# Kernel optimization log

Hardware: AMD Instinct MI355X
Metric: run time of the kernel (lower is better)

Reference implementation:

```python
import jax, jax.numpy as jnp
import numpy as np

N = 50000   # nodes
E = 800000  # edges
D = 128     # hidden_dim == input_dim
H = 8       # heads
C = D // H  # per-head dim = 16
ED = 10     # edge_dim
FF = 4 * D  # ffn hidden = 512


def setup_inputs() -> dict:
    key = jax.random.key(0)
    ks = jax.random.split(key, 20)
    s = 0.05
    p = lambda k, shape: (jax.random.normal(k, shape, jnp.float32) * s)
    return {
        "x": jax.random.normal(ks[0], (N, D), jnp.float32),
        "edge_index": jax.random.randint(ks[1], (2, E), 0, N),
        "edge_attr": jax.random.normal(ks[2], (E, ED), jnp.float32),
        # TransformerConv params (PyG): lin_query/key/value have bias, lin_edge no bias,
        # lin_skip has bias, lin_beta no bias
        "Wq": p(ks[3], (D, D)), "bq": jnp.zeros((D,), jnp.float32),
        "Wk": p(ks[4], (D, D)), "bk": jnp.zeros((D,), jnp.float32),
        "Wv": p(ks[5], (D, D)), "bv": jnp.zeros((D,), jnp.float32),
        "We": p(ks[6], (ED, D)),
        "Wskip": p(ks[7], (D, D)), "bskip": jnp.zeros((D,), jnp.float32),
        "Wbeta": p(ks[8], (3 * D, 1)),
        # GraphNorm params
        "gn_w": jnp.ones((D,), jnp.float32),
        "gn_b": jnp.zeros((D,), jnp.float32),
        "gn_ms": jnp.ones((D,), jnp.float32),  # mean_scale
        # FFN params
        "W1": p(ks[9], (D, FF)), "b1": jnp.zeros((FF,), jnp.float32),
        "W2": p(ks[10], (FF, D)), "b2": jnp.zeros((D,), jnp.float32),
    }


def _layer(x, edge_index, edge_attr, Wq, bq, Wk, bk, Wv, bv, We, Wskip, bskip,
           Wbeta, gn_w, gn_b, gn_ms, W1, b1, W2, b2):
    n = x.shape[0]
    src, dst = edge_index[0], edge_index[1]
    # ---- TransformerConv (concat heads, edge-conditioned, beta skip) ----
    q = (x @ Wq + bq).reshape(n, H, C)
    k = (x @ Wk + bk).reshape(n, H, C)
    v = (x @ Wv + bv).reshape(n, H, C)
    e = (edge_attr @ We).reshape(-1, H, C)          # [E,H,C]
    k_j = k[src] + e                                 # gather + edge bias
    alpha = jnp.einsum('ehc,ehc->eh', q[dst], k_j) / jnp.sqrt(jnp.float32(C))
    # segment softmax over incoming edges of each target node
    amax = jax.ops.segment_max(alpha, dst, num_segments=n)      # [N,H]
    ex = jnp.exp(alpha - amax[dst])
    denom = jax.ops.segment_sum(ex, dst, num_segments=n)        # [N,H]
    alpha = ex / (denom[dst] + 1e-16)
    msg = (v[src] + e) * alpha[:, :, None]           # [E,H,C]
    out = jax.ops.segment_sum(msg.reshape(-1, H * C), dst, num_segments=n)  # [N,D]
    # beta-gated root skip
    x_r = x @ Wskip + bskip
    beta = jax.nn.sigmoid(jnp.concatenate([out, x_r, out - x_r], axis=-1) @ Wbeta)
    x_att = beta * x_r + (1.0 - beta) * out
    # ---- residual + GraphNorm (single graph) ----
    h = x + x_att
    mean = h.mean(axis=0)
    hc = h - gn_ms * mean
    var = (hc * hc).mean(axis=0)
    h = hc / jnp.sqrt(var + 1e-5) * gn_w + gn_b
    # ---- FFN with residual (GELU exact, matching torch default) ----
    ffn = jax.nn.gelu(h @ W1 + b1, approximate=False) @ W2 + b2
    return h + ffn


def reference(x, edge_index, edge_attr, Wq, bq, Wk, bk, Wv, bv, We, Wskip,
              bskip, Wbeta, gn_w, gn_b, gn_ms, W1, b1, W2, b2):
    return _layer(x, edge_index, edge_attr, Wq, bq, Wk, bk, Wv, bv, We, Wskip,
                  bskip, Wbeta, gn_w, gn_b, gn_ms, W1, b1, W2, b2)
```

## Files before the change

### kernel.cpp

```cpp
#include <hip/hip_runtime.h>
#include <hip/hip_fp16.h>
#include <math.h>

#define D 128
#define ED 10
#define FF 512
#define TPAD 520
#define XPAD 136

typedef __attribute__((ext_vector_type(4))) float f32x4;
typedef __attribute__((ext_vector_type(8))) short bf16x8;
using h2 = decltype(__builtin_amdgcn_cvt_pkrtz(0.f, 0.f));
typedef __attribute__((ext_vector_type(2))) float f32x2;

__device__ __forceinline__ ushort f2bf(float f) {
  unsigned u = __float_as_uint(f);
  unsigned r = u + 0x7fffu + ((u >> 16) & 1u);
  return (ushort)(r >> 16);
}
__device__ __forceinline__ float bf2f(ushort u) {
  return __uint_as_float(((unsigned)u) << 16);
}

__device__ __forceinline__ float dpp_add_xor1(float x) {
  int y = __builtin_amdgcn_update_dpp(0, __builtin_bit_cast(int, x), 0xB1, 0xF, 0xF, true);
  return x + __builtin_bit_cast(float, y);
}
__device__ __forceinline__ float dpp_add_xor2(float x) {
  int y = __builtin_amdgcn_update_dpp(0, __builtin_bit_cast(int, x), 0x4E, 0xF, 0xF, true);
  return x + __builtin_bit_cast(float, y);
}

#if __has_builtin(__builtin_amdgcn_cvt_pk_f32_fp8) && __has_builtin(__builtin_amdgcn_cvt_pk_fp8_f32)
#define FP8_HW 1
#else
#define FP8_HW 0
#endif

__device__ __forceinline__ unsigned sw_f2fp8(float f) {
  unsigned u = __float_as_uint(f);
  unsigned s = (u >> 24) & 0x80;
  int e = (int)((u >> 23) & 0xff) - 127;
  unsigned mant = u & 0x7fffff;
  if (e < -9) return s;
  if (e > 8) return s | 0x7e;
  if (e >= -6) {
    unsigned m = mant + 0x7ffff + ((mant >> 20) & 1);
    if (m >= 0x800000) { m = 0; ++e; if (e > 8) return s | 0x7e; }
    return s | ((unsigned)(e + 7) << 3) | (m >> 20);
  }
  unsigned full = 0x800000 | mant;
  int shift = 20 + (-6 - e);
  unsigned m = (full + (1u << (shift - 1)) + ((full >> shift) & 1)) >> shift;
  if (m >= 8) return s | 0x08;
  return s | m;
}
__device__ __forceinline__ float sw_fp82f(unsigned b) {
  unsigned s = (b & 0x80) << 24;
  unsigned e = (b >> 3) & 0xf;
  unsigned m = b & 7;
  if (e == 0) {
    if (m == 0) return __uint_as_float(s);
    float v = (float)(int)m * 0.001953125f;
    return (b & 0x80) ? -v : v;
  }
  return __uint_as_float(s | ((e + 120) << 23) | (m << 20));
}

__device__ __forceinline__ ushort pack_fp8_pair(float a, float b) {
#if FP8_HW
  int r = __builtin_amdgcn_cvt_pk_fp8_f32(a, b, 0, false);
  return (ushort)(r & 0xffff);
#else
  return (ushort)(sw_f2fp8(a) | (sw_f2fp8(b) << 8));
#endif
}
template <bool HI>
__device__ __forceinline__ f32x2 unpack_fp8_pair(unsigned w) {
#if FP8_HW
  auto r = __builtin_amdgcn_cvt_pk_f32_fp8((int)w, HI);
  f32x2 o; o[0] = r[0]; o[1] = r[1];
  return o;
#else
  unsigned v = HI ? (w >> 16) : w;
  f32x2 o; o[0] = sw_fp82f(v & 0xff); o[1] = sw_fp82f((v >> 8) & 0xff);
  return o;
#endif
}

__global__ void prep_hist(const float* __restrict__ Wq, const float* __restrict__ Wk,
                          const float* __restrict__ Wv, const float* __restrict__ Wskip,
                          const float* __restrict__ bq, const float* __restrict__ bk,
                          const float* __restrict__ bv, const float* __restrict__ bskip,
                          const float* __restrict__ W1, const float* __restrict__ W2,
                          const int* __restrict__ dst, int* __restrict__ deg,
                          int* __restrict__ rank, int E,
                          ushort* __restrict__ Wcat_t, float* __restrict__ bcat,
                          ushort* __restrict__ W1t, ushort* __restrict__ W2t) {
  int b = blockIdx.x;
  if (b >= 256) {
    int t = (b - 256) * 256 + threadIdx.x;
    if (t < E) rank[t] = atomicAdd(&deg[dst[t]], 1);
    return;
  }
  int t = b * 256 + threadIdx.x;
  {
    int w = t >> 14, c = (t >> 7) & 127, kk = t & 127;
    const float* W = (w == 0) ? Wq : (w == 1) ? Wk : (w == 2) ? Wv : Wskip;
    Wcat_t[t] = f2bf(W[kk * D + c]);
  }
  {
    int f = t >> 7, kk = t & 127;
    W1t[t] = f2bf(W1[kk * FF + f]);
  }
  {
    int c = t >> 9, f = t & 511;
    W2t[t] = f2bf(W2[f * D + c]);
  }
  if (t < 4 * D) {
    int w = t >> 7;
    const float* bb = (w == 0) ? bq : (w == 1) ? bk : (w == 2) ? bv : bskip;
    bcat[t] = bb[t & 127];
  }
}

__global__ __launch_bounds__(1024) void scan_kernel(const int* __restrict__ deg,
                                                    int* __restrict__ off, int n) {
  __shared__ int part[1024];
  int t = threadIdx.x;
  int chunk = (n + 1023) / 1024;
  int lo = t * chunk, hi = min(lo + chunk, n);
  int s = 0;
  for (int i = lo; i < hi; ++i) s += deg[i];
  part[t] = s;
  __syncthreads();
  for (int dd = 1; dd < 1024; dd <<= 1) {
    int v = (t >= dd) ? part[t - dd] : 0;
    __syncthreads();
    part[t] += v;
    __syncthreads();
  }
  int excl = (t == 0) ? 0 : part[t - 1];
  for (int i = lo; i < hi; ++i) {
    off[i] = excl;
    excl += deg[i];
  }
  if (t == 1023) off[n] = part[1023];
}

__global__ __launch_bounds__(256) void gemm_scatter(
    const float* __restrict__ x, const ushort* __restrict__ Wcat_t,
    const float* __restrict__ bcat, ushort* __restrict__ qb, unsigned* __restrict__ kvf8,
    float* __restrict__ xr, int n, int gm,
    const int* __restrict__ dst, const int* __restrict__ src, const int* __restrict__ rank,
    const int* __restrict__ off, const float* __restrict__ attr,
    unsigned* __restrict__ rec, int E) {
  if ((int)blockIdx.x >= gm) {
    int t = ((int)blockIdx.x - gm) * 256 + threadIdx.x;
    if (t < E) {
      int pos = off[dst[t]] + rank[t];
      const float2* ap = reinterpret_cast<const float2*>(attr + (size_t)t * ED);
      float2 a0 = ap[0], a1 = ap[1], a2 = ap[2], a3 = ap[3], a4 = ap[4];
      unsigned u0 = __builtin_bit_cast(unsigned, __builtin_amdgcn_cvt_pkrtz(a0.x, a0.y));
      unsigned u1 = __builtin_bit_cast(unsigned, __builtin_amdgcn_cvt_pkrtz(a1.x, a1.y));
      unsigned u2 = __builtin_bit_cast(unsigned, __builtin_amdgcn_cvt_pkrtz(a2.x, a2.y));
      unsigned u3 = __builtin_bit_cast(unsigned, __builtin_amdgcn_cvt_pkrtz(a3.x, a3.y));
      unsigned u4 = __builtin_bit_cast(unsigned, __builtin_amdgcn_cvt_pkrtz(a4.x, a4.y));
      uint4* rp = reinterpret_cast<uint4*>(rec + (size_t)pos * 8);
      rp[0] = make_uint4((unsigned)src[t], u0, u1, u2);
      rp[1] = make_uint4(u3, u4, 0u, 0u);
    }
    return;
  }
  __shared__ ushort xa[32 * XPAD];
  int r0 = blockIdx.x * 32;
  {
    int row = threadIdx.x >> 3;
    int seg = threadIdx.x & 7;
    int grow = min(r0 + row, n - 1);
    const float4* p = reinterpret_cast<const float4*>(x + (size_t)grow * D + seg * 16);
    float4 f0 = p[0], f1 = p[1], f2 = p[2], f3 = p[3];
    bf16x8 u0, u1;
    u0[0] = (short)f2bf(f0.x); u0[1] = (short)f2bf(f0.y);
    u0[2] = (short)f2bf(f0.z); u0[3] = (short)f2bf(f0.w);
    u0[4] = (short)f2bf(f1.x); u0[5] = (short)f2bf(f1.y);
    u0[6] = (short)f2bf(f1.z); u0[7] = (short)f2bf(f1.w);
    u1[0] = (short)f2bf(f2.x); u1[1] = (short)f2bf(f2.y);
    u1[2] = (short)f2bf(f2.z); u1[3] = (short)f2bf(f2.w);
    u1[4] = (short)f2bf(f3.x); u1[5] = (short)f2bf(f3.y);
    u1[6] = (short)f2bf(f3.z); u1[7] = (short)f2bf(f3.w);
    ushort* dl = xa + row * XPAD + seg * 16;
    *reinterpret_cast<bf16x8*>(dl) = u0;
    *reinterpret_cast<bf16x8*>(dl + 8) = u1;
  }
  __syncthreads();
  int wv = threadIdx.x >> 6;
  int l = threadIdx.x & 63;
  int lr = l & 15, lg = l >> 4;
  const ushort* Wt = Wcat_t + wv * D * D;
  f32x4 acc[2][8];
#pragma unroll
  for (int m = 0; m < 2; ++m)
#pragma unroll
    for (int nn = 0; nn < 8; ++nn) acc[m][nn] = (f32x4)0.f;
#pragma unroll
  for (int kb2 = 0; kb2 < 4; ++kb2) {
    int k0 = kb2 * 32 + lg * 8;
    bf16x8 a[2];
#pragma unroll
    for (int m = 0; m < 2; ++m)
      a[m] = *reinterpret_cast<const bf16x8*>(xa + (m * 16 + lr) * XPAD + k0);
    bf16x8 b[8];
#pragma unroll
    for (int nn = 0; nn < 8; ++nn)
      b[nn] = *reinterpret_cast<const bf16x8*>(Wt + (nn * 16 + lr) * D + k0);
#pragma unroll
    for (int m = 0; m < 2; ++m)
#pragma unroll
      for (int nn = 0; nn < 8; ++nn)
        acc[m][nn] = __builtin_amdgcn_mfma_f32_16x16x32_bf16(a[m], b[nn], acc[m][nn], 0, 0, 0);
  }
#pragma unroll
  for (int m = 0; m < 2; ++m)
#pragma unroll
    for (int nn = 0; nn < 8; ++nn) {
      int col = nn * 16 + lr;
      float bb = bcat[wv * D + col];
#pragma unroll
      for (int j = 0; j < 4; ++j) {
        int row = r0 + m * 16 + lg * 4 + j;
        float val = acc[m][nn][j] + bb;
        if (wv == 1 || wv == 2) {
          float partner = __shfl_xor(val, 1, 64);
          if (((lr & 1) == 0) && row < n) {
            ushort us = pack_fp8_pair(val, partner);
            size_t idx = ((size_t)row * 64 + nn * 8 + (lr >> 1)) * 2 + (wv - 1);
            reinterpret_cast<ushort*>(kvf8)[idx] = us;
          }
        } else if (row < n) {
          if (wv == 0) qb[(size_t)row * D + col] = f2bf(val);
          else xr[(size_t)row * D + col] = val;
        }
      }
    }
}

__global__ __launch_bounds__(256) void node_attn(
    const unsigned* __restrict__ rec, const int* __restrict__ off,
    const float* __restrict__ We, const ushort* __restrict__ qb,
    const unsigned* __restrict__ kvf8, const float* __restrict__ xr,
    const float* __restrict__ x, const float* __restrict__ Wbeta,
    float* __restrict__ h, float* __restrict__ sums, int n) {
  __shared__ uint4 attrS4[4][64];
  __shared__ unsigned attrS1[4][64];
  __shared__ float rs_h[4 * D], rs_h2[4 * D];
  int wid = threadIdx.x >> 6;
  int l = threadIdx.x & 63;
  int d0 = 2 * l;
  h2 wA[5], wB[5];
#pragma unroll
  for (int t = 0; t < 5; ++t) {
    wA[t] = __builtin_amdgcn_cvt_pkrtz(We[(2 * t) * D + d0], We[(2 * t + 1) * D + d0]);
    wB[t] = __builtin_amdgcn_cvt_pkrtz(We[(2 * t) * D + d0 + 1], We[(2 * t + 1) * D + d0 + 1]);
  }
  float2 wb0 = *reinterpret_cast<const float2*>(Wbeta + d0);
  float2 wb1 = *reinterpret_cast<const float2*>(Wbeta + D + d0);
  float2 wb2 = *reinterpret_cast<const float2*>(Wbeta + 2 * D + d0);
  float s_h0 = 0.f, s_h20 = 0.f, s_h1 = 0.f, s_h21 = 0.f;
  for (int node = blockIdx.x * 4 + wid; node < n; node += gridDim.x * 4) {
    const ushort2 qu = *reinterpret_cast<const ushort2*>(qb + (size_t)node * D + d0);
    float q0 = bf2f(qu.x) * 0.25f, q1 = bf2f(qu.y) * 0.25f;
    int o0 = off[node], dg = off[node + 1] - o0;
    float m = -1e30f, den = 0.f, acc0 = 0.f, acc1 = 0.f;
    for (int chunk = 0; chunk < dg; chunk += 64) {
      int cnt = min(64, dg - chunk);
      long pos = (long)o0 + chunk + l;
      long pend = (long)o0 + dg - 1;
      if (pos > pend) pos = pend;
      const uint4* rp = reinterpret_cast<const uint4*>(rec + (size_t)pos * 8);
      uint4 rA = rp[0], rB = rp[1];
      int s_l = (int)rA.x;
      attrS4[wid][l] = make_uint4(rA.y, rA.z, rA.w, rB.x);
      attrS1[wid][l] = rB.y;
      auto LD = [&](int idx) -> unsigned {
        int ss = __shfl(s_l, idx & 63, 64);
        return kvf8[(size_t)ss * 64 + l];
      };
      auto PROC = [&](unsigned kvw, int i) {
        uint4 av = attrS4[wid][i];
        unsigned av1 = attrS1[wid][i];
        h2 a0 = __builtin_bit_cast(h2, av.x);
        h2 a1 = __builtin_bit_cast(h2, av.y);
        h2 a2 = __builtin_bit_cast(h2, av.z);
        h2 a3 = __builtin_bit_cast(h2, av.w);
        h2 a4 = __builtin_bit_cast(h2, av1);
        float ec0 = __builtin_amdgcn_fdot2(a0, wA[0], 0.f, false);
        ec0 = __builtin_amdgcn_fdot2(a1, wA[1], ec0, false);
        ec0 = __builtin_amdgcn_fdot2(a2, wA[2], ec0, false);
        ec0 = __builtin_amdgcn_fdot2(a3, wA[3], ec0, false);
        ec0 = __builtin_amdgcn_fdot2(a4, wA[4], ec0, false);
        float ec1 = __builtin_amdgcn_fdot2(a0, wB[0], 0.f, false);
        ec1 = __builtin_amdgcn_fdot2(a1, wB[1], ec1, false);
        ec1 = __builtin_amdgcn_fdot2(a2, wB[2], ec1, false);
        ec1 = __builtin_amdgcn_fdot2(a3, wB[3], ec1, false);
        ec1 = __builtin_amdgcn_fdot2(a4, wB[4], ec1, false);
        f32x2 kf = unpack_fp8_pair<false>(kvw);
        f32x2 vf = unpack_fp8_pair<true>(kvw);
        float kk0 = kf[0] + ec0, kk1 = kf[1] + ec1;
        float vv0 = vf[0] + ec0, vv1 = vf[1] + ec1;
        float p = fmaf(q0, kk0, q1 * kk1);
        p = dpp_add_xor1(p);
        p = dpp_add_xor2(p);
        p += __shfl_xor(p, 4, 8);
        if (__any(p > m + 8.f)) {
          float mn = fmaxf(m, p);
          float sc = __expf(m - mn);
          den *= sc; acc0 *= sc; acc1 *= sc;
          m = mn;
        }
        float ex = __expf(p - m);
        den += ex;
        acc0 = fmaf(ex, vv0, acc0);
        acc1 = fmaf(ex, vv1, acc1);
      };
      unsigned p0 = LD(0), p1 = LD(1), p2 = LD(2), p3 = LD(3),
               p4 = LD(4), p5 = LD(5), p6 = LD(6), p7 = LD(7);
      for (int i = 0; i < cnt; i += 8) {
        unsigned c0 = p0, c1 = p1, c2 = p2, c3 = p3, c4 = p4, c5 = p5, c6 = p6, c7 = p7;
        p0 = LD(i + 8);  p1 = LD(i + 9);  p2 = LD(i + 10); p3 = LD(i + 11);
        p4 = LD(i + 12); p5 = LD(i + 13); p6 = LD(i + 14); p7 = LD(i + 15);
        PROC(c0, i);
        if (i + 1 < cnt) PROC(c1, i + 1);
        if (i + 2 < cnt) PROC(c2, i + 2);
        if (i + 3 < cnt) PROC(c3, i + 3);
        if (i + 4 < cnt) PROC(c4, i + 4);
        if (i + 5 < cnt) PROC(c5, i + 5);
        if (i + 6 < cnt) PROC(c6, i + 6);
        if (i + 7 < cnt) PROC(c7, i + 7);
      }
    }
    float inv = 1.f / (den + 1e-16f);
    float oo0 = acc0 * inv, oo1 = acc1 * inv;
    float2 xr2 = *reinterpret_cast<const float2*>(xr + (size_t)node * D + d0);
    float2 x2 = *reinterpret_cast<const float2*>(x + (size_t)node * D + d0);
    float pb = oo0 * wb0.x + xr2.x * wb1.x + (oo0 - xr2.x) * wb2.x
             + oo1 * wb0.y + xr2.y * wb1.y + (oo1 - xr2.y) * wb2.y;
#pragma unroll
    for (int msk = 1; msk < 64; msk <<= 1) pb += __shfl_xor(pb, msk, 64);
    float beta = 1.f / (1.f + __expf(-pb));
    float h0 = x2.x + beta * xr2.x + (1.f - beta) * oo0;
    float h1 = x2.y + beta * xr2.y + (1.f - beta) * oo1;
    *reinterpret_cast<float2*>(h + (size_t)node * D + d0) = make_float2(h0, h1);
    s_h0 += h0; s_h20 += h0 * h0;
    s_h1 += h1; s_h21 += h1 * h1;
  }
  rs_h[wid * D + d0] = s_h0;   rs_h[wid * D + d0 + 1] = s_h1;
  rs_h2[wid * D + d0] = s_h20; rs_h2[wid * D + d0 + 1] = s_h21;
  __syncthreads();
  if (threadIdx.x < D) {
    int d = threadIdx.x;
    float sh = rs_h[d] + rs_h[D + d] + rs_h[2 * D + d] + rs_h[3 * D + d];
    float sh2 = rs_h2[d] + rs_h2[D + d] + rs_h2[2 * D + d] + rs_h2[3 * D + d];
    atomicAdd(&sums[d], sh);
    atomicAdd(&sums[D + d], sh2);
  }
}

__global__ __launch_bounds__(256) void ffn_fused(
    const float* __restrict__ h, const float* __restrict__ sums,
    const float* __restrict__ gn_w, const float* __restrict__ gn_b,
    const float* __restrict__ gn_ms,
    const ushort* __restrict__ W1t, const float* __restrict__ b1,
    const ushort* __restrict__ W2t, const float* __restrict__ b2,
    float* __restrict__ out, float inv_n, int n) {
  __shared__ ushort xa[32 * XPAD];
  __shared__ ushort tt[32 * TPAD];
  __shared__ float scsh[2 * D];
  if (threadIdx.x < D) {
    int d = threadIdx.x;
    float mean = sums[d] * inv_n;
    float ex2 = sums[D + d] * inv_n;
    float ms = gn_ms[d];
    float var = ex2 - 2.f * ms * mean * mean + ms * ms * mean * mean;
    float inv = 1.f / sqrtf(var + 1e-5f);
    float scale = gn_w[d] * inv;
    scsh[d] = scale;
    scsh[D + d] = gn_b[d] - ms * mean * scale;
  }
  __syncthreads();
  int r0 = blockIdx.x * 32;
  {
    int row = threadIdx.x >> 3;
    int seg = threadIdx.x & 7;
    int grow = min(r0 + row, n - 1);
    const float4* p = reinterpret_cast<const float4*>(h + (size_t)grow * D + seg * 16);
    float4 f0 = p[0], f1 = p[1], f2 = p[2], f3 = p[3];
    const float4* sc = reinterpret_cast<const float4*>(scsh + seg * 16);
    const float4* sh = reinterpret_cast<const float4*>(scsh + D + seg * 16);
    float4 s0 = sc[0], s1 = sc[1], s2 = sc[2], s3 = sc[3];
    float4 t0 = sh[0], t1 = sh[1], t2 = sh[2], t3 = sh[3];
    bf16x8 u0, u1;
    u0[0] = (short)f2bf(f0.x * s0.x + t0.x); u0[1] = (short)f2bf(f0.y * s0.y + t0.y);
    u0[2] = (short)f2bf(f0.z * s0.z + t0.z); u0[3] = (short)f2bf(f0.w * s0.w + t0.w);
    u0[4] = (short)f2bf(f1.x * s1.x + t1.x); u0[5] = (short)f2bf(f1.y * s1.y + t1.y);
    u0[6] = (short)f2bf(f1.z * s1.z + t1.z); u0[7] = (short)f2bf(f1.w * s1.w + t1.w);
    u1[0] = (short)f2bf(f2.x * s2.x + t2.x); u1[1] = (short)f2bf(f2.y * s2.y + t2.y);
    u1[2] = (short)f2bf(f2.z * s2.z + t2.z); u1[3] = (short)f2bf(f2.w * s2.w + t2.w);
    u1[4] = (short)f2bf(f3.x * s3.x + t3.x); u1[5] = (short)f2bf(f3.y * s3.y + t3.y);
    u1[6] = (short)f2bf(f3.z * s3.z + t3.z); u1[7] = (short)f2bf(f3.w * s3.w + t3.w);
    ushort* dl = xa + row * XPAD + seg * 16;
    *reinterpret_cast<bf16x8*>(dl) = u0;
    *reinterpret_cast<bf16x8*>(dl + 8) = u1;
  }
  __syncthreads();
  int wv = threadIdx.x >> 6;
  int l = threadIdx.x & 63;
  int lr = l & 15, lg = l >> 4;
  int c0 = wv * 128;
  {
    f32x4 acc[2][8];
#pragma unroll
    for (int m = 0; m < 2; ++m)
#pragma unroll
      for (int nn = 0; nn < 8; ++nn) acc[m][nn] = (f32x4)0.f;
#pragma unroll
    for (int kb = 0; kb < 4; ++kb) {
      int k0 = kb * 32 + lg * 8;
      bf16x8 a[2];
#pragma unroll
      for (int m = 0; m < 2; ++m)
        a[m] = *reinterpret_cast<const bf16x8*>(xa + (m * 16 + lr) * XPAD + k0);
      bf16x8 b[8];
#pragma unroll
      for (int nn = 0; nn < 8; ++nn)
        b[nn] = *reinterpret_cast<const bf16x8*>(W1t + (c0 + nn * 16 + lr) * D + k0);
#pragma unroll
      for (int m = 0; m < 2; ++m)
#pragma unroll
        for (int nn = 0; nn < 8; ++nn)
          acc[m][nn] = __builtin_amdgcn_mfma_f32_16x16x32_bf16(a[m], b[nn], acc[m][nn], 0, 0, 0);
    }
    const float inv_sqrt2 = 0.70710678118654752440f;
#pragma unroll
    for (int m = 0; m < 2; ++m)
#pragma unroll
      for (int nn = 0; nn < 8; ++nn) {
        int col = c0 + nn * 16 + lr;
        float bb = b1[col];
#pragma unroll
        for (int j = 0; j < 4; ++j) {
          int rowl = m * 16 + lg * 4 + j;
          float val = acc[m][nn][j] + bb;
          val = 0.5f * val * (1.f + erff(val * inv_sqrt2));
          tt[rowl * TPAD + col] = f2bf(val);
        }
      }
  }
  __syncthreads();
  {
    f32x4 acc[2][2];
#pragma unroll
    for (int m = 0; m < 2; ++m)
#pragma unroll
      for (int nn = 0; nn < 2; ++nn) acc[m][nn] = (f32x4)0.f;
#pragma unroll 4
    for (int kb = 0; kb < 16; ++kb) {
      int k0 = kb * 32 + lg * 8;
      bf16x8 a[2];
#pragma unroll
      for (int m = 0; m < 2; ++m)
        a[m] = *reinterpret_cast<const bf16x8*>(tt + (m * 16 + lr) * TPAD + k0);
      bf16x8 b[2];
#pragma unroll
      for (int nn = 0; nn < 2; ++nn)
        b[nn] = *reinterpret_cast<const bf16x8*>(W2t + (wv * 32 + nn * 16 + lr) * FF + k0);
#pragma unroll
      for (int m = 0; m < 2; ++m)
#pragma unroll
        for (int nn = 0; nn < 2; ++nn)
          acc[m][nn] = __builtin_amdgcn_mfma_f32_16x16x32_bf16(a[m], b[nn], acc[m][nn], 0, 0, 0);
    }
#pragma unroll
    for (int m = 0; m < 2; ++m)
#pragma unroll
      for (int nn = 0; nn < 2; ++nn) {
        int col = wv * 32 + nn * 16 + lr;
        float bb = b2[col];
#pragma unroll
        for (int j = 0; j < 4; ++j) {
          int rowl = m * 16 + lg * 4 + j;
          int row = r0 + rowl;
          if (row < n) {
            float hn = bf2f(xa[rowl * XPAD + col]);
            out[(size_t)row * D + col] = hn + acc[m][nn][j] + bb;
          }
        }
      }
  }
}

extern "C" void kernel_launch(void* const* d_in, const int* in_sizes, int n_in,
                              void* d_out, int out_size, void* d_ws, size_t ws_size,
                              hipStream_t stream) {
  const float* x     = (const float*)d_in[0];
  const int*   ei    = (const int*)d_in[1];
  const float* attr  = (const float*)d_in[2];
  const float* Wq    = (const float*)d_in[3];
  const float* bq    = (const float*)d_in[4];
  const float* Wk    = (const float*)d_in[5];
  const float* bk    = (const float*)d_in[6];
  const float* Wv    = (const float*)d_in[7];
  const float* bv    = (const float*)d_in[8];
  const float* We    = (const float*)d_in[9];
  const float* Wskip = (const float*)d_in[10];
  const float* bskip = (const float*)d_in[11];
  const float* Wbeta = (const float*)d_in[12];
  const float* gn_w  = (const float*)d_in[13];
  const float* gn_b  = (const float*)d_in[14];
  const float* gn_ms = (const float*)d_in[15];
  const float* W1    = (const float*)d_in[16];
  const float* b1    = (const float*)d_in[17];
  const float* W2    = (const float*)d_in[18];
  const float* b2    = (const float*)d_in[19];

  const int n = in_sizes[0] / D;
  const int E = in_sizes[1] / 2;
  const int* src = ei;
  const int* dst = ei + E;
  const size_t ND = (size_t)n * D;

  ushort* qb = (ushort*)d_ws;
  unsigned* kvf8 = (unsigned*)(qb + ND);
  float* xr = (float*)(kvf8 + (size_t)n * 64);
  int* deg = (int*)(xr + ND);
  float* sums = (float*)(deg + n);
  int* off = (int*)(sums + 2 * D);
  int* rank = off + n + 1;
  unsigned* rec = (unsigned*)(rank + E + 1);
  rec = (unsigned*)(((size_t)rec + 31) & ~(size_t)31);
  ushort* Wcat_t = (ushort*)(rec + (size_t)E * 8);
  ushort* W1t = Wcat_t + 4 * D * D;
  ushort* W2t = W1t + D * FF;
  float* bcat = (float*)(W2t + FF * D);

  (void)hipMemsetAsync(deg, 0, ((size_t)n + 2 * D) * sizeof(int), stream);

  int ghist = (E + 255) / 256;
  prep_hist<<<256 + ghist, 256, 0, stream>>>(Wq, Wk, Wv, Wskip, bq, bk, bv, bskip, W1, W2,
                                             dst, deg, rank, E, Wcat_t, bcat, W1t, W2t);
  scan_kernel<<<1, 1024, 0, stream>>>(deg, off, n);

  int gm = (n + 31) / 32;
  gemm_scatter<<<gm + ghist, 256, 0, stream>>>(x, Wcat_t, bcat, qb, kvf8, xr, n, gm, dst,
                                               src, rank, off, attr, rec, E);

  node_attn<<<2048, 256, 0, stream>>>(rec, off, We, qb, kvf8, xr, x, Wbeta,
                                      (float*)d_out, sums, n);

  ffn_fused<<<(n + 31) / 32, 256, 0, stream>>>((const float*)d_out, sums, gn_w, gn_b, gn_ms,
                                               W1t, b1, W2t, b2, (float*)d_out,
                                               1.f / (float)n, n);
}
```

Before: 377.2 us.

## Factor edge projection out of attention loop via q·We precompute and deferred correction

Instead of computing the 10-dim edge projection e=attr@We for every edge and lane, the kernel precomputes per-head z=We·q once per node so the edge contribution to the score becomes a single fdot2 against that lane's attribute pair. For the value path, it accumulates softmax-weighted raw edge attributes (sat0/sat1) per head group and applies We once after the loop. This removes about ten fdot2 per edge per lane in exchange for extra shuffles per node, a larger LDS layout and some fp16 rounding of the packed z and weighted-sum terms.

```diff
diff --git a/kernel.cpp b/kernel.cpp
--- a/kernel.cpp
+++ b/kernel.cpp
@@ -251,18 +251,21 @@
     const unsigned* __restrict__ kvf8, const float* __restrict__ xr,
     const float* __restrict__ x, const float* __restrict__ Wbeta,
     float* __restrict__ h, float* __restrict__ sums, int n) {
-  __shared__ uint4 attrS4[4][64];
-  __shared__ unsigned attrS1[4][64];
+  __shared__ unsigned attrS[4][64][8];
   __shared__ float rs_h[4 * D], rs_h2[4 * D];
   int wid = threadIdx.x >> 6;
   int l = threadIdx.x & 63;
   int d0 = 2 * l;
-  h2 wA[5], wB[5];
+  int r = l & 7;
+  h2 wA[5], wB[5], wP[10];
 #pragma unroll
   for (int t = 0; t < 5; ++t) {
     wA[t] = __builtin_amdgcn_cvt_pkrtz(We[(2 * t) * D + d0], We[(2 * t + 1) * D + d0]);
     wB[t] = __builtin_amdgcn_cvt_pkrtz(We[(2 * t) * D + d0 + 1], We[(2 * t + 1) * D + d0 + 1]);
   }
+#pragma unroll
+  for (int j = 0; j < 10; ++j)
+    wP[j] = __builtin_amdgcn_cvt_pkrtz(We[j * D + d0], We[j * D + d0 + 1]);
   float2 wb0 = *reinterpret_cast<const float2*>(Wbeta + d0);
   float2 wb1 = *reinterpret_cast<const float2*>(Wbeta + D + d0);
   float2 wb2 = *reinterpret_cast<const float2*>(Wbeta + 2 * D + d0);
@@ -270,8 +273,23 @@
   for (int node = blockIdx.x * 4 + wid; node < n; node += gridDim.x * 4) {
     const ushort2 qu = *reinterpret_cast<const ushort2*>(qb + (size_t)node * D + d0);
     float q0 = bf2f(qu.x) * 0.25f, q1 = bf2f(qu.y) * 0.25f;
+    h2 qpk = __builtin_amdgcn_cvt_pkrtz(q0, q1);
+    float z[10];
+#pragma unroll
+    for (int j = 0; j < 10; ++j) z[j] = __builtin_amdgcn_fdot2(wP[j], qpk, 0.f, false);
+#pragma unroll
+    for (int j = 0; j < 10; ++j) {
+      z[j] = dpp_add_xor1(z[j]);
+      z[j] = dpp_add_xor2(z[j]);
+      z[j] += __shfl_xor(z[j], 4, 8);
+    }
+    float zs0 = (r == 0) ? z[0] : (r == 1) ? z[2] : (r == 2) ? z[4] : (r == 3) ? z[6]
+               : (r == 4) ? z[8] : 0.f;
+    float zs1 = (r == 0) ? z[1] : (r == 1) ? z[3] : (r == 2) ? z[5] : (r == 3) ? z[7]
+               : (r == 4) ? z[9] : 0.f;
+    h2 zqp = __builtin_amdgcn_cvt_pkrtz(zs0, zs1);
     int o0 = off[node], dg = off[node + 1] - o0;
-    float m = -1e30f, den = 0.f, acc0 = 0.f, acc1 = 0.f;
+    float m = -1e30f, den = 0.f, acc0 = 0.f, acc1 = 0.f, sat0 = 0.f, sat1 = 0.f;
     for (int chunk = 0; chunk < dg; chunk += 64) {
       int cnt = min(64, dg - chunk);
       long pos = (long)o0 + chunk + l;
@@ -280,48 +298,35 @@
       const uint4* rp = reinterpret_cast<const uint4*>(rec + (size_t)pos * 8);
       uint4 rA = rp[0], rB = rp[1];
       int s_l = (int)rA.x;
-      attrS4[wid][l] = make_uint4(rA.y, rA.z, rA.w, rB.x);
-      attrS1[wid][l] = rB.y;
+      uint4* asl = reinterpret_cast<uint4*>(&attrS[wid][l][0]);
+      asl[0] = make_uint4(rA.y, rA.z, rA.w, rB.x);
+      asl[1] = make_uint4(rB.y, rB.z, rB.w, 0u);
       auto LD = [&](int idx) -> unsigned {
         int ss = __shfl(s_l, idx & 63, 64);
         return kvf8[(size_t)ss * 64 + l];
       };
       auto PROC = [&](unsigned kvw, int i) {
-        uint4 av = attrS4[wid][i];
-        unsigned av1 = attrS1[wid][i];
-        h2 a0 = __builtin_bit_cast(h2, av.x);
-        h2 a1 = __builtin_bit_cast(h2, av.y);
-        h2 a2 = __builtin_bit_cast(h2, av.z);
-        h2 a3 = __builtin_bit_cast(h2, av.w);
-        h2 a4 = __builtin_bit_cast(h2, av1);
-        float ec0 = __builtin_amdgcn_fdot2(a0, wA[0], 0.f, false);
-        ec0 = __builtin_amdgcn_fdot2(a1, wA[1], ec0, false);
-        ec0 = __builtin_amdgcn_fdot2(a2, wA[2], ec0, false);
-        ec0 = __builtin_amdgcn_fdot2(a3, wA[3], ec0, false);
-        ec0 = __builtin_amdgcn_fdot2(a4, wA[4], ec0, false);
-        float ec1 = __builtin_amdgcn_fdot2(a0, wB[0], 0.f, false);
-        ec1 = __builtin_amdgcn_fdot2(a1, wB[1], ec1, false);
-        ec1 = __builtin_amdgcn_fdot2(a2, wB[2], ec1, false);
-        ec1 = __builtin_amdgcn_fdot2(a3, wB[3], ec1, false);
-        ec1 = __builtin_amdgcn_fdot2(a4, wB[4], ec1, false);
+        h2 at = __builtin_bit_cast(h2, attrS[wid][i][r]);
         f32x2 kf = unpack_fp8_pair<false>(kvw);
         f32x2 vf = unpack_fp8_pair<true>(kvw);
-        float kk0 = kf[0] + ec0, kk1 = kf[1] + ec1;
-        float vv0 = vf[0] + ec0, vv1 = vf[1] + ec1;
-        float p = fmaf(q0, kk0, q1 * kk1);
+        float p = fmaf(q0, kf[0], q1 * kf[1]);
+        p = __builtin_amdgcn_fdot2(at, zqp, p, false);
         p = dpp_add_xor1(p);
         p = dpp_add_xor2(p);
         p += __shfl_xor(p, 4, 8);
         if (__any(p > m + 8.f)) {
           float mn = fmaxf(m, p);
           float sc = __expf(m - mn);
-          den *= sc; acc0 *= sc; acc1 *= sc;
+          den *= sc; acc0 *= sc; acc1 *= sc; sat0 *= sc; sat1 *= sc;
           m = mn;
         }
         float ex = __expf(p - m);
         den += ex;
-        acc0 = fmaf(ex, vv0, acc0);
-        acc1 = fmaf(ex, vv1, acc1);
+        acc0 = fmaf(ex, vf[0], acc0);
+        acc1 = fmaf(ex, vf[1], acc1);
+        float atf0 = (float)at[0], atf1 = (float)at[1];
+        sat0 = fmaf(ex, atf0, sat0);
+        sat1 = fmaf(ex, atf1, sat1);
       };
       unsigned p0 = LD(0), p1 = LD(1), p2 = LD(2), p3 = LD(3),
                p4 = LD(4), p5 = LD(5), p6 = LD(6), p7 = LD(7);
@@ -339,8 +344,22 @@
         if (i + 7 < cnt) PROC(c7, i + 7);
       }
     }
+    int base = l & ~7;
+    h2 Spk[5];
+#pragma unroll
+    for (int t = 0; t < 5; ++t) {
+      float a = __shfl(sat0, base + t, 64);
+      float b = __shfl(sat1, base + t, 64);
+      Spk[t] = __builtin_amdgcn_cvt_pkrtz(a, b);
+    }
+    float corr0 = 0.f, corr1 = 0.f;
+#pragma unroll
+    for (int t = 0; t < 5; ++t) {
+      corr0 = __builtin_amdgcn_fdot2(Spk[t], wA[t], corr0, false);
+      corr1 = __builtin_amdgcn_fdot2(Spk[t], wB[t], corr1, false);
+    }
     float inv = 1.f / (den + 1e-16f);
-    float oo0 = acc0 * inv, oo1 = acc1 * inv;
+    float oo0 = (acc0 + corr0) * inv, oo1 = (acc1 + corr1) * inv;
     float2 xr2 = *reinterpret_cast<const float2*>(xr + (size_t)node * D + d0);
     float2 x2 = *reinterpret_cast<const float2*>(x + (size_t)node * D + d0);
     float pb = oo0 * wb0.x + xr2.x * wb1.x + (oo0 - xr2.x) * wb2.x
```

Result: no change. 378.6 us (+0.4%).
